# Kernel optimization log

Measured on AMD Instinct MI355X. Metric: run time of the kernel, lower is better.

## Reference

```python
import jax, jax.numpy as jnp
import numpy as np

MARGIN = 2.0
EPS = 1e-9


def setup_inputs() -> dict:
    key = jax.random.key(0)
    k1, k2 = jax.random.split(key)
    N, D, C = 8192, 128, 50
    outputs = jax.random.normal(k1, (N, D), dtype=jnp.float32)
    labels = jax.random.randint(k2, (N,), 0, C, dtype=jnp.int64)
    return {"outputs": outputs, "labels": labels}


def reference(outputs, labels):
    # Pairwise squared distances via Gram trick: ||xi||^2 + ||xj||^2 - 2 xi.xj
    sq = jnp.sum(outputs * outputs, axis=-1)  # [N]
    gram = outputs @ outputs.T                # [N, N]
    dist_sq = jnp.maximum(sq[:, None] + sq[None, :] - 2.0 * gram, 0.0)

    pos = (labels[:, None] == labels[None, :])  # includes i==j, as in original
    num_pos = jnp.sum(pos)
    num_neg = pos.size - num_pos

    dist_pos = jnp.sum(jnp.where(pos, dist_sq, 0.0))
    hinge = jax.nn.relu(MARGIN - jnp.sqrt(dist_sq + EPS))
    dist_neg = jnp.sum(jnp.where(pos, 0.0, hinge * hinge))

    pos_term = jnp.where(num_pos > 0, 0.5 * dist_pos / num_pos, 0.0)
    neg_term = jnp.where(num_neg > 0, 0.5 * dist_neg / num_neg, 0.0)
    return pos_term + neg_term
```

## Files before the change

kernel.cpp:

```cpp
#include <hip/hip_runtime.h>
#include <math.h>

#define NPTS   8192
#define DDIM   128
#define NBLK   64
#define NTRI   2080
#define TPB    4
#define GRID   (NTRI / TPB)

using short8 = __attribute__((ext_vector_type(8))) short;
using f32x4  = __attribute__((ext_vector_type(4))) float;

__device__ __forceinline__ unsigned short f2bf(float f) {
    unsigned int u = __float_as_uint(f);
    u += 0x7fffu + ((u >> 16) & 1u);
    return (unsigned short)(u >> 16);
}
__device__ __forceinline__ float bf2f(unsigned short s) {
    return __uint_as_float(((unsigned int)s) << 16);
}

__device__ __forceinline__ void gld_lds16(const unsigned short* g, unsigned short* l) {
    __builtin_amdgcn_global_load_lds(
        (const __attribute__((address_space(1))) unsigned int*)g,
        (__attribute__((address_space(3))) unsigned int*)l,
        16, 0, 0);
}

__global__ __launch_bounds__(256) void prep_kernel(
    const float* __restrict__ X, unsigned short* __restrict__ Xbf,
    float* __restrict__ sq)
{
    const int wave = threadIdx.x >> 6, lane = threadIdx.x & 63;
    const int row  = blockIdx.x * 4 + wave;
    float2 v = *(const float2*)(X + (size_t)row * DDIM + lane * 2);
    unsigned short a = f2bf(v.x), b = f2bf(v.y);
    float fa = bf2f(a), fb = bf2f(b);
    float s = fa * fa + fb * fb;
    *(ushort2*)(Xbf + (size_t)row * DDIM + lane * 2) = make_ushort2(a, b);
#pragma unroll
    for (int off = 32; off > 0; off >>= 1) s += __shfl_down(s, off);
    if (lane == 0) sq[row] = s;
}

__global__ __launch_bounds__(256) void pair_kernel(
    const unsigned short* __restrict__ Xbf, const int* __restrict__ lab,
    const float* __restrict__ sq, float* __restrict__ slots )
{
    const int k0 = blockIdx.x * TPB;
    int bi = (int)((129.0f - sqrtf((float)(16641 - 8 * k0))) * 0.5f);
    if (bi < 0) bi = 0;
    while (64 * (bi + 1) - ((bi + 1) * bi) / 2 <= k0) ++bi;
    while (64 * bi - (bi * (bi - 1)) / 2 > k0) --bi;
    int bj = bi + (k0 - (64 * bi - (bi * (bi - 1)) / 2));

    __shared__ unsigned short tile[65536];
    __shared__ float sSqA[128], sSqB[128];
    __shared__ int   sLabA[128], sLabB[128];
    __shared__ float rP[4], rN[4];

    const int tid  = threadIdx.x;
    const int rloc = tid >> 4;
    const int cswz = ((tid & 15) ^ (rloc & 7)) * 8;
    const int lws  = (tid & ~63) * 8;

    auto stage = [&](int row0, int panel) {
        const unsigned short* g = Xbf + (size_t)(row0 + rloc) * DDIM + cswz;
        unsigned short* l = &tile[panel * 16384 + lws];
#pragma unroll
        for (int i = 0; i < 8; ++i)
            gld_lds16(g + (size_t)i * 16 * DDIM, l + i * 2048);
    };

    int aCur = 0;
    stage(bi * 128, 0);
    stage(bj * 128, 2);

    const int wave = tid >> 6, lane = tid & 63;
    const int quad = lane >> 4, rr = lane & 15;
    const int wr = wave >> 1, wc = wave & 1;
    const int r7 = rr & 7;

    int bi_c = bi, bj_c = bj;

#pragma unroll
    for (int t = 0; t < TPB; ++t) {
        const int rowA0 = bi_c * 128, rowB0 = bj_c * 128;

        float sqv; int labv;
        {
            int r = (tid < 128) ? (rowA0 + tid) : (rowB0 + (tid - 128));
            sqv  = sq[r];
            labv = lab[r];
        }

        int bi_n = bi_c, bj_n = bj_c + 1;
        if (bj_n == NBLK) { bi_n = bi_c + 1; bj_n = bi_n; }
        int aNext = aCur;

        if (t < TPB - 1) {
            if (bi_n != bi_c) {
                aNext = aCur ^ 1;
                stage(bi_n * 128, aNext);
                stage(bj_n * 128, 2 + ((t + 1) & 1));
                asm volatile("s_waitcnt vmcnt(16)" ::: "memory");
            } else {
                stage(bj_n * 128, 2 + ((t + 1) & 1));
                asm volatile("s_waitcnt vmcnt(8)" ::: "memory");
            }
        } else {
            asm volatile("s_waitcnt vmcnt(0)" ::: "memory");
        }

        if (tid < 128) { sSqA[tid] = sqv;      sLabA[tid] = labv; }
        else           { sSqB[tid - 128] = sqv; sLabB[tid - 128] = labv; }
        asm volatile("s_waitcnt lgkmcnt(0)" ::: "memory");
        __builtin_amdgcn_s_barrier();
        __builtin_amdgcn_sched_barrier(0);

        const unsigned short* tA = &tile[aCur * 16384 + (size_t)(wr * 64 + rr) * 128];
        const unsigned short* tB = &tile[(2 + (t & 1)) * 16384 + (size_t)(wc * 64 + rr) * 128];

        f32x4 acc[4][4];
#pragma unroll
        for (int i = 0; i < 4; ++i)
#pragma unroll
            for (int j = 0; j < 4; ++j)
                acc[i][j] = (f32x4){0.f, 0.f, 0.f, 0.f};

#pragma unroll
        for (int kc = 0; kc < 4; ++kc) {
            const int s = (((kc * 4 + quad) ^ r7)) * 8;
            short8 a[4], b[4];
#pragma unroll
            for (int u = 0; u < 4; ++u)
                a[u] = *(const short8*)(tA + u * 16 * 128 + s);
#pragma unroll
            for (int u = 0; u < 4; ++u)
                b[u] = *(const short8*)(tB + u * 16 * 128 + s);
#pragma unroll
            for (int i = 0; i < 4; ++i)
#pragma unroll
                for (int j = 0; j < 4; ++j)
                    acc[i][j] = __builtin_amdgcn_mfma_f32_16x16x32_bf16(a[i], b[j], acc[i][j], 0, 0, 0);
        }

        float sb[4]; int lbv[4];
#pragma unroll
        for (int j = 0; j < 4; ++j) {
            int cl = wc * 64 + j * 16 + rr;
            sb[j]  = sSqB[cl];
            lbv[j] = sLabB[cl];
        }

        float posS = 0.f, dmin = 1e30f;
#pragma unroll
        for (int i = 0; i < 4; ++i) {
#pragma unroll
            for (int rg = 0; rg < 4; ++rg) {
                int   rl = wr * 64 + i * 16 + quad * 4 + rg;
                float sa = sSqA[rl];
                int   la = sLabA[rl];
#pragma unroll
                for (int j = 0; j < 4; ++j) {
                    float d = fmaxf(sa + sb[j] - 2.0f * acc[i][j][rg], 0.0f);
                    bool same = (la == lbv[j]);
                    posS += same ? d : 0.f;
                    dmin = fminf(dmin, same ? 1e30f : d);
                }
            }
        }

        float negS = 0.f;
        if (__any(dmin + 1e-9f < 4.0f)) {
#pragma unroll
            for (int i = 0; i < 4; ++i) {
#pragma unroll
                for (int rg = 0; rg < 4; ++rg) {
                    int   rl = wr * 64 + i * 16 + quad * 4 + rg;
                    float sa = sSqA[rl];
                    int   la = sLabA[rl];
#pragma unroll
                    for (int j = 0; j < 4; ++j) {
                        float d = fmaxf(sa + sb[j] - 2.0f * acc[i][j][rg], 0.0f);
                        float h = fmaxf(2.0f - sqrtf(d + 1e-9f), 0.f);
                        negS += (la == lbv[j]) ? 0.f : h * h;
                    }
                }
            }
        }

        const float factor = (bi_c == bj_c) ? 1.0f : 2.0f;
        posS *= factor; negS *= factor;

#pragma unroll
        for (int off = 32; off > 0; off >>= 1) {
            posS += __shfl_down(posS, off);
            negS += __shfl_down(negS, off);
        }
        if (lane == 0) { rP[wave] = posS; rN[wave] = negS; }
        asm volatile("s_waitcnt lgkmcnt(0)" ::: "memory");
        __builtin_amdgcn_s_barrier();
        __builtin_amdgcn_sched_barrier(0);
        if (tid == 0) {
            slots[k0 + t]        = rP[0] + rP[1] + rP[2] + rP[3];
            slots[NTRI + k0 + t] = rN[0] + rN[1] + rN[2] + rN[3];
        }

        bi_c = bi_n; bj_c = bj_n; aCur = aNext;
    }
}

__global__ __launch_bounds__(1024) void finalize_kernel(
    const float* __restrict__ slots, const int* __restrict__ lab,
    float* __restrict__ out)
{
    __shared__ int   hist[64];
    __shared__ float sP[16], sN[16];
    const int tid = threadIdx.x;
    if (tid < 64) hist[tid] = 0;
    __syncthreads();
    for (int i = tid; i < NPTS; i += 1024) atomicAdd(&hist[lab[i]], 1);

    float p = 0.f, n = 0.f;
    for (int i = tid; i < NTRI; i += 1024) { p += slots[i]; n += slots[NTRI + i]; }
#pragma unroll
    for (int off = 32; off > 0; off >>= 1) {
        p += __shfl_down(p, off);
        n += __shfl_down(n, off);
    }
    const int wave = tid >> 6, lane = tid & 63;
    if (lane == 0) { sP[wave] = p; sN[wave] = n; }
    __syncthreads();
    if (tid == 0) {
        long long np = 0;
        for (int c = 0; c < 64; ++c) np += (long long)hist[c] * hist[c];
        float tp = 0.f, tn = 0.f;
#pragma unroll
        for (int w = 0; w < 16; ++w) { tp += sP[w]; tn += sN[w]; }
        double dnp = (double)np;
        double dnn = (double)NPTS * (double)NPTS - dnp;
        double pt = (dnp > 0.0) ? 0.5 * (double)tp / dnp : 0.0;
        double nt = (dnn > 0.0) ? 0.5 * (double)tn / dnn : 0.0;
        out[0] = (float)(pt + nt);
    }
}

extern "C" void kernel_launch(void* const* d_in, const int* in_sizes, int n_in,
                              void* d_out, int out_size, void* d_ws, size_t ws_size,
                              hipStream_t stream) {
    const float* X   = (const float*)d_in[0];
    const int*   lab = (const int*)d_in[1];
    float*       out = (float*)d_out;

    char* ws = (char*)d_ws;
    unsigned short* Xbf   = (unsigned short*)(ws);
    float*          sq    = (float*)(ws + 2 * 1024 * 1024);
    float*          slots = (float*)(ws + 2 * 1024 * 1024 + 32 * 1024);

    prep_kernel<<<NPTS / 4, 256, 0, stream>>>(X, Xbf, sq);
    pair_kernel<<<GRID, 256, 0, stream>>>(Xbf, lab, sq, slots);
    finalize_kernel<<<1, 1024, 0, stream>>>(slots, lab, out);
}
```

Before: 101.5 us.

## Halve LDS tile by prefetching next B panel into registers instead of LDS

Shrinks the shared tile from four panels to two. The next B panel is prefetched through registers during compute and written to LDS after the reduction barrier, and A is restaged synchronously only when the row block changes. The goal is lower LDS usage, so more blocks can be resident per CU, while still hiding the global loads for B. The costs are extra VGPR pressure from eight short8 registers and an exposed stall whenever the A panel changes.

```diff
diff --git a/kernel.cpp b/kernel.cpp
--- a/kernel.cpp
+++ b/kernel.cpp
@@ -54,7 +54,7 @@
     while (64 * bi - (bi * (bi - 1)) / 2 > k0) --bi;
     int bj = bi + (k0 - (64 * bi - (bi * (bi - 1)) / 2));
 
-    __shared__ unsigned short tile[65536];
+    __shared__ unsigned short tile[32768];
     __shared__ float sSqA[128], sSqB[128];
     __shared__ int   sLabA[128], sLabB[128];
     __shared__ float rP[4], rN[4];
@@ -64,62 +64,55 @@
     const int cswz = ((tid & 15) ^ (rloc & 7)) * 8;
     const int lws  = (tid & ~63) * 8;
 
-    auto stage = [&](int row0, int panel) {
+    auto stage = [&](int row0, int panelBase) {
         const unsigned short* g = Xbf + (size_t)(row0 + rloc) * DDIM + cswz;
-        unsigned short* l = &tile[panel * 16384 + lws];
+        unsigned short* l = &tile[panelBase + lws];
 #pragma unroll
         for (int i = 0; i < 8; ++i)
             gld_lds16(g + (size_t)i * 16 * DDIM, l + i * 2048);
     };
 
-    int aCur = 0;
     stage(bi * 128, 0);
-    stage(bj * 128, 2);
+    stage(bj * 128, 16384);
+    {
+        int r = (tid < 128) ? (bi * 128 + tid) : (bj * 128 + (tid - 128));
+        float sv = sq[r]; int lv = lab[r];
+        if (tid < 128) { sSqA[tid] = sv;        sLabA[tid] = lv; }
+        else           { sSqB[tid - 128] = sv;  sLabB[tid - 128] = lv; }
+    }
+    __syncthreads();
 
     const int wave = tid >> 6, lane = tid & 63;
     const int quad = lane >> 4, rr = lane & 15;
     const int wr = wave >> 1, wc = wave & 1;
-    const int r7 = rr & 7;
+    const int r7 = rr & 15 & 7;
+
+    const unsigned short* tA = &tile[(size_t)(wr * 64 + rr) * 128];
+    const unsigned short* tB = &tile[16384 + (size_t)(wc * 64 + rr) * 128];
+
+    const int wrow = tid >> 4;
+    const int wswz = (tid & 15) ^ (wrow & 7);
 
     int bi_c = bi, bj_c = bj;
 
 #pragma unroll
     for (int t = 0; t < TPB; ++t) {
-        const int rowA0 = bi_c * 128, rowB0 = bj_c * 128;
-
-        float sqv; int labv;
-        {
-            int r = (tid < 128) ? (rowA0 + tid) : (rowB0 + (tid - 128));
-            sqv  = sq[r];
-            labv = lab[r];
-        }
-
+        const bool last = (t == TPB - 1);
         int bi_n = bi_c, bj_n = bj_c + 1;
         if (bj_n == NBLK) { bi_n = bi_c + 1; bj_n = bi_n; }
-        int aNext = aCur;
-
-        if (t < TPB - 1) {
-            if (bi_n != bi_c) {
-                aNext = aCur ^ 1;
-                stage(bi_n * 128, aNext);
-                stage(bj_n * 128, 2 + ((t + 1) & 1));
-                asm volatile("s_waitcnt vmcnt(16)" ::: "memory");
-            } else {
-                stage(bj_n * 128, 2 + ((t + 1) & 1));
-                asm volatile("s_waitcnt vmcnt(8)" ::: "memory");
-            }
-        } else {
-            asm volatile("s_waitcnt vmcnt(0)" ::: "memory");
-        }
-
-        if (tid < 128) { sSqA[tid] = sqv;      sLabA[tid] = labv; }
-        else           { sSqB[tid - 128] = sqv; sLabB[tid - 128] = labv; }
-        asm volatile("s_waitcnt lgkmcnt(0)" ::: "memory");
-        __builtin_amdgcn_s_barrier();
-        __builtin_amdgcn_sched_barrier(0);
-
-        const unsigned short* tA = &tile[aCur * 16384 + (size_t)(wr * 64 + rr) * 128];
-        const unsigned short* tB = &tile[(2 + (t & 1)) * 16384 + (size_t)(wc * 64 + rr) * 128];
+        const bool aChg = (bi_n != bi_c);
+
+        short8 rB[8];
+        float sqN = 0.f; int labN = 0;
+        if (!last) {
+            const unsigned short* gB = Xbf + (size_t)bj_n * 128 * DDIM + tid * 8;
+#pragma unroll
+            for (int c = 0; c < 8; ++c)
+                rB[c] = *(const short8*)(gB + c * 2048);
+            if (tid >= 128)   { sqN = sq[bj_n * 128 + tid - 128]; labN = lab[bj_n * 128 + tid - 128]; }
+            else if (aChg)    { sqN = sq[bi_n * 128 + tid];       labN = lab[bi_n * 128 + tid]; }
+            __builtin_amdgcn_sched_barrier(0);
+        }
 
         f32x4 acc[4][4];
 #pragma unroll
@@ -199,15 +192,34 @@
             negS += __shfl_down(negS, off);
         }
         if (lane == 0) { rP[wave] = posS; rN[wave] = negS; }
+
         asm volatile("s_waitcnt lgkmcnt(0)" ::: "memory");
         __builtin_amdgcn_s_barrier();
         __builtin_amdgcn_sched_barrier(0);
+
         if (tid == 0) {
             slots[k0 + t]        = rP[0] + rP[1] + rP[2] + rP[3];
             slots[NTRI + k0 + t] = rN[0] + rN[1] + rN[2] + rN[3];
         }
 
-        bi_c = bi_n; bj_c = bj_n; aCur = aNext;
+        if (!last) {
+            asm volatile("s_waitcnt vmcnt(0)" ::: "memory");
+#pragma unroll
+            for (int c = 0; c < 8; ++c)
+                *(short8*)(&tile[16384 + (size_t)(c * 16 + wrow) * 128 + wswz * 8]) = rB[c];
+            if (tid >= 128)   { sSqB[tid - 128] = sqN; sLabB[tid - 128] = labN; }
+            else if (aChg)    { sSqA[tid] = sqN;       sLabA[tid] = labN; }
+            if (aChg) {
+                stage(bi_n * 128, 0);
+                asm volatile("s_waitcnt vmcnt(0) lgkmcnt(0)" ::: "memory");
+            } else {
+                asm volatile("s_waitcnt lgkmcnt(0)" ::: "memory");
+            }
+            __builtin_amdgcn_s_barrier();
+            __builtin_amdgcn_sched_barrier(0);
+        }
+
+        bi_c = bi_n; bj_c = bj_n;
     }
 }
 
```

Result: slower. 104.6 us (+3.1%).
